# Kernel optimization log

Measured on AMD Instinct MI355X. Metric: run time of the kernel, lower is better.

The kernel has to match this reference:

```python
import math
import jax, jax.numpy as jnp
import numpy as np

B, T, C = 2, 2048, 1024
N_HEAD = 16
HEAD_DIM = C // N_HEAD

def setup_inputs() -> dict:
    key = jax.random.key(0)
    kx, kq, kk, kv, kp = jax.random.split(key, 5)
    s = 1.0 / math.sqrt(C)
    return {
        "x": jax.random.normal(kx, (B, T, C), dtype=jnp.float32),
        "Wq": jax.random.normal(kq, (C, C), dtype=jnp.float32) * s,
        "Wk": jax.random.normal(kk, (C, C), dtype=jnp.float32) * s,
        "Wv": jax.random.normal(kv, (C, C), dtype=jnp.float32) * s,
        "Wproj": jax.random.normal(kp, (C, C), dtype=jnp.float32) * s,
    }

def reference(x, Wq, Wk, Wv, Wproj):
    b, t, c = x.shape
    # nn.Linear(no bias): x @ W.T ; weights stored [out, in]
    def heads(w):
        return (x @ w.T).reshape(b, t, N_HEAD, HEAD_DIM).transpose(0, 2, 1, 3)  # [B,H,T,D]
    q, k, v = heads(Wq), heads(Wk), heads(Wv)
    att = jnp.einsum('bhqd,bhkd->bhqk', q, k) / math.sqrt(HEAD_DIM)  # [B,H,T,T]
    causal = jnp.tril(jnp.ones((t, t), dtype=bool))
    att = jnp.where(causal, att, -jnp.inf)
    att = jax.nn.softmax(att, axis=-1)
    y = jnp.einsum('bhqk,bhkd->bhqd', att, v)           # [B,H,T,D]
    y = y.transpose(0, 2, 1, 3).reshape(b, t, c)        # [B,T,C]
    return y @ Wproj.T
```

## Files before the change

### kernel.cpp

```cpp
#include <hip/hip_runtime.h>
#include <stdint.h>

typedef uint16_t u16;
typedef uint32_t u32;
typedef __attribute__((ext_vector_type(8))) _Float16 f16x8;
typedef __attribute__((ext_vector_type(4))) _Float16 f16x4;
typedef __attribute__((ext_vector_type(4))) float f32x4;
typedef __attribute__((ext_vector_type(2))) uint32_t u32x2;

#define NB 2
#define NT 2048
#define NC 1024
#define NH 16
#define ND 64
#define NM (NB*NT)
#define LOG2E 1.44269504088896340736f
#define PSTRIDE 4352

__device__ __forceinline__ u16 f2h(float f) {
  _Float16 h = (_Float16)f;
  return __builtin_bit_cast(u16, h);
}

__global__ __launch_bounds__(256) void cvt_kernel(const float* __restrict__ src,
                                                  u16* __restrict__ dst, int n4) {
  int i = blockIdx.x * 256 + threadIdx.x;
  if (i >= n4) return;
  float4 v = ((const float4*)src)[i];
  ushort4 o;
  o.x = f2h(v.x); o.y = f2h(v.y); o.z = f2h(v.z); o.w = f2h(v.w);
  ((ushort4*)dst)[i] = o;
}

__global__ __launch_bounds__(256) void cvtw_kernel(const float* __restrict__ w0,
                                                   const float* __restrict__ w1,
                                                   const float* __restrict__ w2,
                                                   const float* __restrict__ w3,
                                                   u16* __restrict__ dst) {
  int i = blockIdx.x * 256 + threadIdx.x;
  int which = i >> 18;
  const float* src = (which == 0) ? w0 : (which == 1) ? w1 : (which == 2) ? w2 : w3;
  int j = i & 262143;
  float4 v = ((const float4*)src)[j];
  ushort4 o;
  o.x = f2h(v.x); o.y = f2h(v.y); o.z = f2h(v.z); o.w = f2h(v.w);
  ((ushort4*)dst)[i] = o;
}

__device__ __forceinline__ void gload16(const void* g, void* l) {
  __builtin_amdgcn_global_load_lds(
      (const __attribute__((address_space(1))) void*)g,
      (__attribute__((address_space(3))) void*)l, 16, 0, 0);
}

template<int EPI>
__global__ __launch_bounds__(256) void gemm_bt(const u16* __restrict__ A,
                                               const u16* __restrict__ Bw,
                                               int K, int N,
                                               u16* __restrict__ oq, u16* __restrict__ okk,
                                               u16* __restrict__ ovt,
                                               float* __restrict__ of) {
  __shared__ __align__(16) u16 SH[4*128*64];
  u16* Al = SH;
  u16* Bl = SH + 2*128*64;
  const int tid = threadIdx.x, lane = tid & 63, wid = tid >> 6;
  const int g = lane >> 4, qq = lane & 15;
  const int wm = wid >> 1, wn = wid & 1;
  const int m0 = blockIdx.y * 128, n0 = blockIdx.x * 128;
  const int srow = lane >> 3;
  const int scol8 = (lane & 7) ^ srow;

  f32x4 acc[4][4] = {};
  const int nk = K >> 6;

  #pragma unroll
  for (int pp = 0; pp < 4; ++pp) {
    int r = wid*32 + pp*8;
    gload16(A  + (size_t)(m0 + r + srow)*K + scol8*8, &Al[r*64]);
    gload16(Bw + (size_t)(n0 + r + srow)*K + scol8*8, &Bl[r*64]);
  }

  for (int kt = 0; kt < nk; ++kt) {
    const int cur = kt & 1;
    __syncthreads();
    if (kt + 1 < nk) {
      const int k1 = (kt + 1) << 6;
      #pragma unroll
      for (int pp = 0; pp < 4; ++pp) {
        int r = wid*32 + pp*8;
        gload16(A  + (size_t)(m0 + r + srow)*K + k1 + scol8*8, &Al[(cur^1)*8192 + r*64]);
        gload16(Bw + (size_t)(n0 + r + srow)*K + k1 + scol8*8, &Bl[(cur^1)*8192 + r*64]);
      }
    }
    #pragma unroll
    for (int kk = 0; kk < 2; ++kk) {
      f16x8 af[4], bfr[4];
      #pragma unroll
      for (int mt = 0; mt < 4; ++mt) {
        int row = wm*64 + mt*16 + qq;
        af[mt] = *(const f16x8*)&Al[cur*8192 + row*64 + (((kk*4 + g) ^ (qq & 7))*8)];
      }
      #pragma unroll
      for (int nt = 0; nt < 4; ++nt) {
        int row = wn*64 + nt*16 + qq;
        bfr[nt] = *(const f16x8*)&Bl[cur*8192 + row*64 + (((kk*4 + g) ^ (qq & 7))*8)];
      }
      #pragma unroll
      for (int mt = 0; mt < 4; ++mt)
        #pragma unroll
        for (int nt = 0; nt < 4; ++nt)
          acc[mt][nt] = __builtin_amdgcn_mfma_f32_16x16x32_f16(af[mt], bfr[nt], acc[mt][nt], 0, 0, 0);
    }
  }

  if (EPI == 0) {
    __syncthreads();
    u16* reg = SH + wid*4096;
    const int sel = n0 >> 10;
    const int h = ((n0 & 1023) >> 6) + wn;
    const int bq = m0 >> 11;

    if (sel < 2) {
      const float scale = (sel == 0) ? 0.125f*LOG2E : 1.0f;
      #pragma unroll
      for (int mt = 0; mt < 4; ++mt)
        #pragma unroll
        for (int r = 0; r < 4; ++r) {
          int mloc = mt*16 + g*4 + r;
          #pragma unroll
          for (int nt = 0; nt < 4; ++nt) {
            int d = nt*16 + qq;
            reg[mloc*64 + (d ^ (g << 4))] = f2h(acc[mt][nt][r] * scale);
          }
        }
      u16* dst = (sel == 0) ? oq : okk;
      const int slot = lane & 7;
      #pragma unroll
      for (int i = 0; i < 8; ++i) {
        int row = i*8 + (lane >> 3);
        int physslot = slot ^ (((row >> 2) & 3) << 1);
        f16x8 vvv = *(const f16x8*)&reg[row*64 + physslot*8];
        int m = m0 + wm*64 + row;
        int t = m & (NT-1);
        *(f16x8*)(dst + (((size_t)(bq*NH + h)*NT + t)*ND) + slot*8) = vvv;
      }
    } else {
      #pragma unroll
      for (int nt = 0; nt < 4; ++nt) {
        int d = nt*16 + qq;
        int f = (d & 7) << 3;
        #pragma unroll
        for (int mt = 0; mt < 4; ++mt)
          #pragma unroll
          for (int rp = 0; rp < 2; ++rp) {
            int r = rp*2;
            int mloc = mt*16 + g*4 + r;
            u32 pk = (u32)f2h(acc[mt][nt][r]) | ((u32)f2h(acc[mt][nt][r+1]) << 16);
            *(u32*)&reg[d*64 + (mloc ^ f)] = pk;
          }
      }
      const int slot = lane & 7;
      const int t0 = m0 + wm*64;
      #pragma unroll
      for (int i = 0; i < 8; ++i) {
        int d = i*8 + (lane >> 3);
        int physslot = slot ^ (d & 7);
        f16x8 vvv = *(const f16x8*)&reg[d*64 + physslot*8];
        int t = (t0 & (NT-1)) + slot*8;
        *(f16x8*)(ovt + ((size_t)(bq*NH + h)*ND + d)*NT + t) = vvv;
      }
    }
  } else {
    #pragma unroll
    for (int mt = 0; mt < 4; ++mt)
      #pragma unroll
      for (int r = 0; r < 4; ++r) {
        int m = m0 + wm*64 + mt*16 + g*4 + r;
        #pragma unroll
        for (int nt = 0; nt < 4; ++nt) {
          int n = n0 + wn*64 + nt*16 + qq;
          of[(size_t)m*N + n] = acc[mt][nt][r];
        }
      }
  }
}

#define IT(q,s,c,m) ((u32)(q) | ((u32)(s)<<8) | ((u32)(c)<<16) | ((u32)(m)<<24))
__global__ __launch_bounds__(256, 5) void attn_kernel(const u16* __restrict__ q,
                                                      const u16* __restrict__ k,
                                                      const u16* __restrict__ vt,
                                                      u16* __restrict__ y,
                                                      u16* __restrict__ part) {
  static const u32 items[60] = {
    IT(11,0,12,0),  IT(22,0,12,21), IT(23,0,12,23), IT(23,12,12,24),
    IT(10,0,11,0),  IT(20,0,11,17), IT(21,0,11,19), IT(21,11,11,20),
    IT(22,12,11,22),IT(30,0,11,43), IT(31,0,11,46), IT(31,11,11,47),
    IT(9,0,10,0),   IT(18,0,10,13), IT(19,0,10,15), IT(19,10,10,16),
    IT(20,11,10,18),IT(27,0,10,34), IT(28,0,10,37), IT(28,10,10,38),
    IT(29,0,10,40), IT(29,10,10,41),IT(29,20,10,42),IT(30,11,10,44),
    IT(30,21,10,45),IT(31,22,10,48),
    IT(8,0,9,0),    IT(16,0,9,9),   IT(17,0,9,11),  IT(17,9,9,12),
    IT(18,10,9,14), IT(24,0,9,25),  IT(25,0,9,28),  IT(25,9,9,29),
    IT(26,0,9,31),  IT(26,9,9,32),  IT(26,18,9,33), IT(27,10,9,35),
    IT(27,19,9,36), IT(28,20,9,39),
    IT(7,0,8,0),    IT(14,0,8,5),   IT(15,0,8,7),   IT(15,8,8,8),
    IT(16,9,8,10),  IT(24,9,8,26),  IT(24,17,8,27), IT(25,18,8,30),
    IT(6,0,7,0),    IT(12,0,7,1),   IT(13,0,7,3),   IT(13,7,7,4),
    IT(14,8,7,6),
    IT(5,0,6,0),    IT(12,7,6,2),
    IT(4,0,5,0), IT(3,0,4,0), IT(2,0,3,0), IT(1,0,2,0), IT(0,0,1,0)
  };
  __shared__ __align__(16) u16 Kl[2][64*64];
  __shared__ __align__(16) u16 Vl[2][64*64];
  const int tid = threadIdx.x, lane = tid & 63, wid = tid >> 6;
  const int g = lane >> 4, qq = lane & 15;
  const int bh = blockIdx.x;
  const u32 it = items[blockIdx.y];
  const int qtile = it & 255;
  const int ks = (it >> 8) & 255;
  const int kc = (it >> 16) & 255;
  const int mode = it >> 24;
  const int qs = qtile * 64;
  const u16* qp = q  + (size_t)bh*NT*ND;
  const u16* kp = k  + (size_t)bh*NT*ND;
  const u16* vp = vt + (size_t)bh*ND*NT;
  const int b = bh >> 4, h = bh & 15;
  const int srow = lane >> 3;
  const int scol8 = (lane & 7) ^ (srow & 7);

  f16x8 aq[2];
  {
    int t = qs + wid*16 + qq;
    #pragma unroll
    for (int c = 0; c < 2; ++c)
      aq[c] = *(const f16x8*)(qp + (size_t)t*ND + c*32 + 8*g);
  }

  f16x4 ones4;
  #pragma unroll
  for (int i = 0; i < 4; ++i) ones4[i] = (_Float16)1.0f;

  f32x4 accO[4] = {};
  f32x4 accS = {};
  float m_run = -1e30f;

  #pragma unroll
  for (int pp = 0; pp < 2; ++pp) {
    int issue = wid*2 + pp;
    int row = issue*8 + srow;
    gload16(kp + (size_t)(ks*64 + row)*ND + scol8*8, &Kl[0][issue*512]);
    gload16(vp + (size_t)row*NT + ks*64 + scol8*8, &Vl[0][issue*512]);
  }

  for (int kt = ks; kt < ks + kc; ++kt) {
    const int kvs = kt*64;
    const int cur = (kt - ks) & 1;
    __syncthreads();

    if (kt + 1 < ks + kc) {
      const int kvs2 = kvs + 64;
      #pragma unroll
      for (int pp = 0; pp < 2; ++pp) {
        int issue = wid*2 + pp;
        int row = issue*8 + srow;
        gload16(kp + (size_t)(kvs2 + row)*ND + scol8*8, &Kl[cur^1][issue*512]);
        gload16(vp + (size_t)row*NT + kvs2 + scol8*8, &Vl[cur^1][issue*512]);
      }
    }

    f32x4 sacc[4] = {};
    __builtin_amdgcn_s_setprio(1);
    #pragma unroll
    for (int c = 0; c < 2; ++c) {
      #pragma unroll
      for (int nt = 0; nt < 4; ++nt) {
        int row = nt*16 + qq;
        int col = (c*32 + 8*g) ^ ((row & 7) << 3);
        f16x8 kb = *(const f16x8*)&Kl[cur][row*64 + col];
        sacc[nt] = __builtin_amdgcn_mfma_f32_16x16x32_f16(kb, aq[c], sacc[nt], 0, 0, 0);
      }
    }
    __builtin_amdgcn_s_setprio(0);

    if (kvs + 63 > qs + wid*16) {
      int qg = qs + wid*16 + qq;
      #pragma unroll
      for (int nt = 0; nt < 4; ++nt)
        #pragma unroll
        for (int r = 0; r < 4; ++r)
          if (kvs + nt*16 + g*4 + r > qg) sacc[nt][r] = -1e30f;
    }

    float m0a = fmaxf(fmaxf(sacc[0][0], sacc[0][1]), fmaxf(sacc[0][2], sacc[0][3]));
    float m1a = fmaxf(fmaxf(sacc[1][0], sacc[1][1]), fmaxf(sacc[1][2], sacc[1][3]));
    float m2a = fmaxf(fmaxf(sacc[2][0], sacc[2][1]), fmaxf(sacc[2][2], sacc[2][3]));
    float m3a = fmaxf(fmaxf(sacc[3][0], sacc[3][1]), fmaxf(sacc[3][2], sacc[3][3]));
    float mloc = fmaxf(fmaxf(m0a, m1a), fmaxf(m2a, m3a));

    const bool defer = __all(mloc <= m_run + 8.f);
    float mnew;
    if (defer) {
      mnew = m_run;
    } else {
      float mf = fmaxf(mloc, __shfl_xor(mloc, 16));
      mf = fmaxf(mf, __shfl_xor(mf, 32));
      mnew = fmaxf(m_run, mf);
      float a = exp2f(m_run - mnew);
      m_run = mnew;
      #pragma unroll
      for (int dt = 0; dt < 4; ++dt) accO[dt] *= a;
      accS *= a;
    }

    f16x4 pb[4];
    #pragma unroll
    for (int nt = 0; nt < 4; ++nt) {
      float p0 = exp2f(sacc[nt][0] - mnew);
      float p1 = exp2f(sacc[nt][1] - mnew);
      float p2 = exp2f(sacc[nt][2] - mnew);
      float p3 = exp2f(sacc[nt][3] - mnew);
      u32x2 w;
      w.x = __builtin_bit_cast(u32, __builtin_amdgcn_cvt_pkrtz(p0, p1));
      w.y = __builtin_bit_cast(u32, __builtin_amdgcn_cvt_pkrtz(p2, p3));
      pb[nt] = __builtin_bit_cast(f16x4, w);
    }

    __builtin_amdgcn_s_setprio(1);
    #pragma unroll
    for (int nt = 0; nt < 4; ++nt) {
      accS = __builtin_amdgcn_mfma_f32_16x16x16f16(ones4, pb[nt], accS, 0, 0, 0);
      #pragma unroll
      for (int dt = 0; dt < 4; ++dt) {
        int vrow = dt*16 + qq;
        int slot = (2*nt + (g >> 1)) ^ (vrow & 7);
        f16x4 vb = *(const f16x4*)&Vl[cur][vrow*64 + slot*8 + (g & 1)*4];
        accO[dt] = __builtin_amdgcn_mfma_f32_16x16x16f16(vb, pb[nt], accO[dt], 0, 0, 0);
      }
    }
    __builtin_amdgcn_s_setprio(0);
  }

  const float inv = 1.0f / accS[0];
  if (mode == 0) {
    int t = qs + wid*16 + qq;
    #pragma unroll
    for (int dt = 0; dt < 4; ++dt) {
      u32x2 st;
      st.x = (u32)f2h(accO[dt][0]*inv) | ((u32)f2h(accO[dt][1]*inv) << 16);
      st.y = (u32)f2h(accO[dt][2]*inv) | ((u32)f2h(accO[dt][3]*inv) << 16);
      *(u32x2*)(y + ((size_t)(b*NT + t))*NC + h*ND + dt*16 + g*4) = st;
    }
  } else {
    const int slot = bh*48 + (mode - 1);
    u16* pp = part + (size_t)slot * PSTRIDE;
    float* hd = (float*)(pp + 4096);
    const int rloc = wid*16 + qq;
    #pragma unroll
    for (int dt = 0; dt < 4; ++dt) {
      u32x2 st;
      st.x = (u32)f2h(accO[dt][0]*inv) | ((u32)f2h(accO[dt][1]*inv) << 16);
      st.y = (u32)f2h(accO[dt][2]*inv) | ((u32)f2h(accO[dt][3]*inv) << 16);
      *(u32x2*)(pp + rloc*64 + dt*16 + g*4) = st;
    }
    if (g == 0) { hd[rloc] = m_run; hd[64 + rloc] = accS[0]; }
  }
}

__global__ __launch_bounds__(256) void combine_kernel(const u16* __restrict__ part,
                                                      u16* __restrict__ y) {
  const int qtile = 12 + blockIdx.x;
  const int bh = blockIdx.y;
  const int b = bh >> 4, h = bh & 15;
  const int nc = (qtile < 24) ? 2 : 3;
  const int pbase = (qtile < 24) ? (qtile - 12)*2 : 24 + (qtile - 24)*3;
  const u16* p0 = part + (size_t)(bh*48 + pbase) * PSTRIDE;
  const int tid = threadIdx.x;
  const int d0 = (tid & 7) * 8;
  #pragma unroll
  for (int i = 0; i < 2; ++i) {
    int r = (tid >> 3) + 32*i;
    float m0 = ((const float*)(p0 + 4096))[r];
    float l0 = ((const float*)(p0 + 4096))[64 + r];
    float m1 = ((const float*)(p0 + PSTRIDE + 4096))[r];
    float l1 = ((const float*)(p0 + PSTRIDE + 4096))[64 + r];
    float m2 = (nc == 3) ? ((const float*)(p0 + 2*PSTRIDE + 4096))[r]      : -1e30f;
    float l2 = (nc == 3) ? ((const float*)(p0 + 2*PSTRIDE + 4096))[64 + r] : 0.f;
    float mm = fmaxf(fmaxf(m0, m1), m2);
    float w0 = exp2f(m0 - mm) * l0;
    float w1 = exp2f(m1 - mm) * l1;
    float w2 = exp2f(m2 - mm) * l2;
    float inv = 1.0f / (w0 + w1 + w2);
    float a0 = w0 * inv, a1 = w1 * inv, a2 = w2 * inv;
    f16x8 o0 = *(const f16x8*)&p0[r*64 + d0];
    f16x8 o1 = *(const f16x8*)&p0[PSTRIDE + r*64 + d0];
    f16x8 o2 = *(const f16x8*)&p0[2*PSTRIDE + r*64 + d0];
    f16x8 out;
    #pragma unroll
    for (int e = 0; e < 8; ++e)
      out[e] = (_Float16)(a0*(float)o0[e] + a1*(float)o1[e] + a2*(float)o2[e]);
    int t = qtile*64 + r;
    *(f16x8*)(y + ((size_t)(b*NT + t))*NC + h*ND + d0) = out;
  }
}

extern "C" void kernel_launch(void* const* d_in, const int* in_sizes, int n_in,
                              void* d_out, int out_size, void* d_ws, size_t ws_size,
                              hipStream_t stream) {
  const float* x  = (const float*)d_in[0];
  const float* Wq = (const float*)d_in[1];
  const float* Wk = (const float*)d_in[2];
  const float* Wv = (const float*)d_in[3];
  const float* Wp = (const float*)d_in[4];

  u16* xb   = (u16*)d_ws;
  u16* wqkv = xb   + (size_t)NM*NC;
  u16* wpj  = wqkv + (size_t)3*NC*NC;
  u16* qb   = wpj  + (size_t)NC*NC;
  u16* kb   = qb   + (size_t)NM*NC;
  u16* vtb  = kb   + (size_t)NM*NC;
  u16* yb   = vtb  + (size_t)NM*NC;
  u16* part = xb;
  size_t need = ((size_t)NM*NC*5 + (size_t)4*NC*NC) * sizeof(u16);
  if (ws_size < need) return;

  cvt_kernel<<<NM*NC/4/256, 256, 0, stream>>>(x, xb, NM*NC/4);
  cvtw_kernel<<<4*NC*NC/4/256, 256, 0, stream>>>(Wq, Wk, Wv, Wp, wqkv);

  gemm_bt<0><<<dim3(3*NC/128, NM/128), 256, 0, stream>>>(xb, wqkv, NC, 3*NC,
                                                         qb, kb, vtb, nullptr);
  attn_kernel<<<dim3(NB*NH, 60), 256, 0, stream>>>(qb, kb, vtb, yb, part);
  combine_kernel<<<dim3(20, NB*NH), 256, 0, stream>>>(part, yb);
  gemm_bt<1><<<dim3(NC/128, NM/128), 256, 0, stream>>>(yb, wpj, NC, NC,
                                                       nullptr, nullptr, nullptr,
                                                       (float*)d_out);
}
```

Baseline: 112.0 us.

## Double attention query tile to 128 rows with 8-wave blocks and merged conversion

The attention kernel now processes 128 query rows per block with 512 threads (8 waves). Each K/V tile staged in LDS is therefore reused by twice as many queries, and the number of work items and split partials drops by half. The work-item schedule, partial-slot layout and combine kernel are rewritten to match the 128-row tiles. The two fp32-to-fp16 conversion kernels are also merged into one launch. The larger blocks and the new launch bounds may raise register pressure or reduce scheduling flexibility. Causal load balance across blocks also becomes coarser.

Result: slower. 128.0 us (+14.3%).

```diff
diff --git a/kernel.cpp b/kernel.cpp
--- a/kernel.cpp
+++ b/kernel.cpp
@@ -15,36 +15,41 @@
 #define ND 64
 #define NM (NB*NT)
 #define LOG2E 1.44269504088896340736f
-#define PSTRIDE 4352
+#define PSTRIDE 8704
 
 __device__ __forceinline__ u16 f2h(float f) {
   _Float16 h = (_Float16)f;
   return __builtin_bit_cast(u16, h);
 }
 
-__global__ __launch_bounds__(256) void cvt_kernel(const float* __restrict__ src,
-                                                  u16* __restrict__ dst, int n4) {
+__global__ __launch_bounds__(256) void cvt_all(const float* __restrict__ x,
+                                               const float* __restrict__ w0,
+                                               const float* __restrict__ w1,
+                                               const float* __restrict__ w2,
+                                               const float* __restrict__ w3,
+                                               u16* __restrict__ xb,
+                                               u16* __restrict__ wdst) {
   int i = blockIdx.x * 256 + threadIdx.x;
-  if (i >= n4) return;
-  float4 v = ((const float4*)src)[i];
-  ushort4 o;
-  o.x = f2h(v.x); o.y = f2h(v.y); o.z = f2h(v.z); o.w = f2h(v.w);
-  ((ushort4*)dst)[i] = o;
-}
-
-__global__ __launch_bounds__(256) void cvtw_kernel(const float* __restrict__ w0,
-                                                   const float* __restrict__ w1,
-                                                   const float* __restrict__ w2,
-                                                   const float* __restrict__ w3,
-                                                   u16* __restrict__ dst) {
-  int i = blockIdx.x * 256 + threadIdx.x;
-  int which = i >> 18;
-  const float* src = (which == 0) ? w0 : (which == 1) ? w1 : (which == 2) ? w2 : w3;
-  int j = i & 262143;
+  const int XTOT = NM*NC/4;
+  const float* src;
+  u16* dst;
+  int j;
+  if (i < XTOT) { src = x; dst = xb; j = i; }
+  else {
+    j = i - XTOT;
+    int which = j >> 18;
+    src = (which == 0) ? w0 : (which == 1) ? w1 : (which == 2) ? w2 : w3;
+    dst = wdst;
+    float4 v = ((const float4*)src)[j & 262143];
+    ushort4 o;
+    o.x = f2h(v.x); o.y = f2h(v.y); o.z = f2h(v.z); o.w = f2h(v.w);
+    ((ushort4*)dst)[j] = o;
+    return;
+  }
   float4 v = ((const float4*)src)[j];
   ushort4 o;
   o.x = f2h(v.x); o.y = f2h(v.y); o.z = f2h(v.z); o.w = f2h(v.w);
-  ((ushort4*)dst)[i] = o;
+  ((ushort4*)dst)[j] = o;
 }
 
 __device__ __forceinline__ void gload16(const void* g, void* l) {
@@ -186,29 +191,21 @@
 }
 
 #define IT(q,s,c,m) ((u32)(q) | ((u32)(s)<<8) | ((u32)(c)<<16) | ((u32)(m)<<24))
-__global__ __launch_bounds__(256, 5) void attn_kernel(const u16* __restrict__ q,
+__global__ __launch_bounds__(512, 8) void attn_kernel(const u16* __restrict__ q,
                                                       const u16* __restrict__ k,
                                                       const u16* __restrict__ vt,
                                                       u16* __restrict__ y,
                                                       u16* __restrict__ part) {
-  static const u32 items[60] = {
-    IT(11,0,12,0),  IT(22,0,12,21), IT(23,0,12,23), IT(23,12,12,24),
-    IT(10,0,11,0),  IT(20,0,11,17), IT(21,0,11,19), IT(21,11,11,20),
-    IT(22,12,11,22),IT(30,0,11,43), IT(31,0,11,46), IT(31,11,11,47),
-    IT(9,0,10,0),   IT(18,0,10,13), IT(19,0,10,15), IT(19,10,10,16),
-    IT(20,11,10,18),IT(27,0,10,34), IT(28,0,10,37), IT(28,10,10,38),
-    IT(29,0,10,40), IT(29,10,10,41),IT(29,20,10,42),IT(30,11,10,44),
-    IT(30,21,10,45),IT(31,22,10,48),
-    IT(8,0,9,0),    IT(16,0,9,9),   IT(17,0,9,11),  IT(17,9,9,12),
-    IT(18,10,9,14), IT(24,0,9,25),  IT(25,0,9,28),  IT(25,9,9,29),
-    IT(26,0,9,31),  IT(26,9,9,32),  IT(26,18,9,33), IT(27,10,9,35),
-    IT(27,19,9,36), IT(28,20,9,39),
-    IT(7,0,8,0),    IT(14,0,8,5),   IT(15,0,8,7),   IT(15,8,8,8),
-    IT(16,9,8,10),  IT(24,9,8,26),  IT(24,17,8,27), IT(25,18,8,30),
-    IT(6,0,7,0),    IT(12,0,7,1),   IT(13,0,7,3),   IT(13,7,7,4),
-    IT(14,8,7,6),
-    IT(5,0,6,0),    IT(12,7,6,2),
-    IT(4,0,5,0), IT(3,0,4,0), IT(2,0,3,0), IT(1,0,2,0), IT(0,0,1,0)
+  static const u32 items[30] = {
+    IT(11,0,12,11), IT(11,12,12,12), IT(5,0,12,0),
+    IT(15,0,11,22), IT(15,11,11,23), IT(10,0,11,9), IT(10,11,11,10),
+    IT(15,22,10,24), IT(14,0,10,19), IT(14,10,10,20), IT(14,20,10,21),
+    IT(13,0,10,16),  IT(9,0,10,7),   IT(9,10,10,8),  IT(4,0,10,0),
+    IT(13,10,9,17), IT(13,19,9,18), IT(12,0,9,13), IT(12,9,9,14),
+    IT(8,0,9,5),    IT(8,9,9,6),
+    IT(12,18,8,15), IT(7,0,8,3), IT(7,8,8,4), IT(3,0,8,0),
+    IT(6,0,7,1), IT(6,7,7,2),
+    IT(2,0,6,0), IT(1,0,4,0), IT(0,0,2,0)
   };
   __shared__ __align__(16) u16 Kl[2][64*64];
   __shared__ __align__(16) u16 Vl[2][64*64];
@@ -220,13 +217,13 @@
   const int ks = (it >> 8) & 255;
   const int kc = (it >> 16) & 255;
   const int mode = it >> 24;
-  const int qs = qtile * 64;
+  const int qs = qtile * 128;
   const u16* qp = q  + (size_t)bh*NT*ND;
   const u16* kp = k  + (size_t)bh*NT*ND;
   const u16* vp = vt + (size_t)bh*ND*NT;
   const int b = bh >> 4, h = bh & 15;
-  const int srow = lane >> 3;
-  const int scol8 = (lane & 7) ^ (srow & 7);
+  const int strow = tid >> 3;
+  const int stcol = (tid & 7) ^ (strow & 7);
 
   f16x8 aq[2];
   {
@@ -244,13 +241,8 @@
   f32x4 accS = {};
   float m_run = -1e30f;
 
-  #pragma unroll
-  for (int pp = 0; pp < 2; ++pp) {
-    int issue = wid*2 + pp;
-    int row = issue*8 + srow;
-    gload16(kp + (size_t)(ks*64 + row)*ND + scol8*8, &Kl[0][issue*512]);
-    gload16(vp + (size_t)row*NT + ks*64 + scol8*8, &Vl[0][issue*512]);
-  }
+  gload16(kp + (size_t)(ks*64 + strow)*ND + stcol*8, &Kl[0][wid*512]);
+  gload16(vp + (size_t)strow*NT + ks*64 + stcol*8, &Vl[0][wid*512]);
 
   for (int kt = ks; kt < ks + kc; ++kt) {
     const int kvs = kt*64;
@@ -259,13 +251,8 @@
 
     if (kt + 1 < ks + kc) {
       const int kvs2 = kvs + 64;
-      #pragma unroll
-      for (int pp = 0; pp < 2; ++pp) {
-        int issue = wid*2 + pp;
-        int row = issue*8 + srow;
-        gload16(kp + (size_t)(kvs2 + row)*ND + scol8*8, &Kl[cur^1][issue*512]);
-        gload16(vp + (size_t)row*NT + kvs2 + scol8*8, &Vl[cur^1][issue*512]);
-      }
+      gload16(kp + (size_t)(kvs2 + strow)*ND + stcol*8, &Kl[cur^1][wid*512]);
+      gload16(vp + (size_t)strow*NT + kvs2 + stcol*8, &Vl[cur^1][wid*512]);
     }
 
     f32x4 sacc[4] = {};
@@ -351,9 +338,9 @@
       *(u32x2*)(y + ((size_t)(b*NT + t))*NC + h*ND + dt*16 + g*4) = st;
     }
   } else {
-    const int slot = bh*48 + (mode - 1);
+    const int slot = bh*24 + (mode - 1);
     u16* pp = part + (size_t)slot * PSTRIDE;
-    float* hd = (float*)(pp + 4096);
+    float* hd = (float*)(pp + 8192);
     const int rloc = wid*16 + qq;
     #pragma unroll
     for (int dt = 0; dt < 4; ++dt) {
@@ -362,29 +349,29 @@
       st.y = (u32)f2h(accO[dt][2]*inv) | ((u32)f2h(accO[dt][3]*inv) << 16);
       *(u32x2*)(pp + rloc*64 + dt*16 + g*4) = st;
     }
-    if (g == 0) { hd[rloc] = m_run; hd[64 + rloc] = accS[0]; }
+    if (g == 0) { hd[rloc] = m_run; hd[128 + rloc] = accS[0]; }
   }
 }
 
 __global__ __launch_bounds__(256) void combine_kernel(const u16* __restrict__ part,
                                                       u16* __restrict__ y) {
-  const int qtile = 12 + blockIdx.x;
+  const int qtile = 6 + blockIdx.x;
   const int bh = blockIdx.y;
   const int b = bh >> 4, h = bh & 15;
-  const int nc = (qtile < 24) ? 2 : 3;
-  const int pbase = (qtile < 24) ? (qtile - 12)*2 : 24 + (qtile - 24)*3;
-  const u16* p0 = part + (size_t)(bh*48 + pbase) * PSTRIDE;
+  const int nc = (qtile < 12) ? 2 : 3;
+  const int pbase = (qtile < 12) ? (qtile - 6)*2 : 12 + (qtile - 12)*3;
+  const u16* p0 = part + (size_t)(bh*24 + pbase) * PSTRIDE;
   const int tid = threadIdx.x;
   const int d0 = (tid & 7) * 8;
   #pragma unroll
-  for (int i = 0; i < 2; ++i) {
+  for (int i = 0; i < 4; ++i) {
     int r = (tid >> 3) + 32*i;
-    float m0 = ((const float*)(p0 + 4096))[r];
-    float l0 = ((const float*)(p0 + 4096))[64 + r];
-    float m1 = ((const float*)(p0 + PSTRIDE + 4096))[r];
-    float l1 = ((const float*)(p0 + PSTRIDE + 4096))[64 + r];
-    float m2 = (nc == 3) ? ((const float*)(p0 + 2*PSTRIDE + 4096))[r]      : -1e30f;
-    float l2 = (nc == 3) ? ((const float*)(p0 + 2*PSTRIDE + 4096))[64 + r] : 0.f;
+    float m0 = ((const float*)(p0 + 8192))[r];
+    float l0 = ((const float*)(p0 + 8192))[128 + r];
+    float m1 = ((const float*)(p0 + PSTRIDE + 8192))[r];
+    float l1 = ((const float*)(p0 + PSTRIDE + 8192))[128 + r];
+    float m2 = (nc == 3) ? ((const float*)(p0 + 2*PSTRIDE + 8192))[r]       : -1e30f;
+    float l2 = (nc == 3) ? ((const float*)(p0 + 2*PSTRIDE + 8192))[128 + r] : 0.f;
     float mm = fmaxf(fmaxf(m0, m1), m2);
     float w0 = exp2f(m0 - mm) * l0;
     float w1 = exp2f(m1 - mm) * l1;
@@ -398,7 +385,7 @@
     #pragma unroll
     for (int e = 0; e < 8; ++e)
       out[e] = (_Float16)(a0*(float)o0[e] + a1*(float)o1[e] + a2*(float)o2[e]);
-    int t = qtile*64 + r;
+    int t = qtile*128 + r;
     *(f16x8*)(y + ((size_t)(b*NT + t))*NC + h*ND + d0) = out;
   }
 }
@@ -423,13 +410,12 @@
   size_t need = ((size_t)NM*NC*5 + (size_t)4*NC*NC) * sizeof(u16);
   if (ws_size < need) return;
 
-  cvt_kernel<<<NM*NC/4/256, 256, 0, stream>>>(x, xb, NM*NC/4);
-  cvtw_kernel<<<4*NC*NC/4/256, 256, 0, stream>>>(Wq, Wk, Wv, Wp, wqkv);
+  cvt_all<<<(NM*NC/4 + 4*NC*NC/4)/256, 256, 0, stream>>>(x, Wq, Wk, Wv, Wp, xb, wqkv);
 
   gemm_bt<0><<<dim3(3*NC/128, NM/128), 256, 0, stream>>>(xb, wqkv, NC, 3*NC,
                                                          qb, kb, vtb, nullptr);
-  attn_kernel<<<dim3(NB*NH, 60), 256, 0, stream>>>(qb, kb, vtb, yb, part);
-  combine_kernel<<<dim3(20, NB*NH), 256, 0, stream>>>(part, yb);
+  attn_kernel<<<dim3(NB*NH, 30), 512, 0, stream>>>(qb, kb, vtb, yb, part);
+  combine_kernel<<<dim3(10, NB*NH), 256, 0, stream>>>(part, yb);
   gemm_bt<1><<<dim3(NC/128, NM/128), 256, 0, stream>>>(yb, wpj, NC, NC,
                                                        nullptr, nullptr, nullptr,
                                                        (float*)d_out);
```
